# Optimization experiments

Hardware: AMD Instinct MI355X
Metric: run time of the kernel (lower is better)

Reference implementation:

```python
import jax, jax.numpy as jnp
import numpy as np

D_MODEL = 1024
NUM_HEADS = 16
DK = D_MODEL // NUM_HEADS
THETA = 10000.0
B, S = 4, 2048


def _rope(x, pos):
    # x: [B, H, S, dk], pos: [S] int positions
    half = DK // 2
    inv_freq = THETA ** (-jnp.arange(half, dtype=jnp.float32) * 2.0 / DK)  # [half]
    ang = pos.astype(jnp.float32)[:, None] * inv_freq[None, :]             # [S, half]
    cos, sin = jnp.cos(ang), jnp.sin(ang)                                  # [S, half]
    x_even = x[..., 0::2]
    x_odd = x[..., 1::2]
    out_even = x_even * cos - x_odd * sin
    out_odd = x_even * sin + x_odd * cos
    # interleave back to [..., dk]
    return jnp.stack([out_even, out_odd], axis=-1).reshape(x.shape)


def setup_inputs() -> dict:
    key = jax.random.key(0)
    ks = jax.random.split(key, 5)
    scale = 1.0 / np.sqrt(D_MODEL)
    return {
        "x": jax.random.normal(ks[0], (B, S, D_MODEL), dtype=jnp.float32),
        "token_position": jnp.arange(S, dtype=jnp.int32),
        "wq": jax.random.normal(ks[1], (D_MODEL, D_MODEL), dtype=jnp.float32) * scale,
        "wk": jax.random.normal(ks[2], (D_MODEL, D_MODEL), dtype=jnp.float32) * scale,
        "wv": jax.random.normal(ks[3], (D_MODEL, D_MODEL), dtype=jnp.float32) * scale,
        "wo": jax.random.normal(ks[4], (D_MODEL, D_MODEL), dtype=jnp.float32) * scale,
    }


def reference(x, token_position, wq, wk, wv, wo):
    b, s, _ = x.shape
    # QKV projections (torch Linear: y = x @ W.T), split heads -> [B, H, S, dk]
    def proj(w):
        y = jnp.einsum("bsd,ed->bse", x, w)
        return y.reshape(b, s, NUM_HEADS, DK).transpose(0, 2, 1, 3)
    q, k, v = proj(wq), proj(wk), proj(wv)
    q = _rope(q, token_position)
    k = _rope(k, token_position)
    # causal SDPA
    scores = jnp.einsum("bhqd,bhkd->bhqk", q, k) / jnp.sqrt(jnp.float32(DK))
    causal = jnp.tril(jnp.ones((s, s), dtype=bool))
    scores = jnp.where(causal, scores, -jnp.inf)
    attn = jax.nn.softmax(scores, axis=-1)
    out = jnp.einsum("bhqk,bhkd->bhqd", attn, v)          # [B, H, S, dv]
    out = out.transpose(0, 2, 1, 3).reshape(b, s, D_MODEL)  # merge heads
    return jnp.einsum("bsd,ed->bse", out, wo)             # output projection
```

## Files before the change

### kernel.cpp

```cpp
#include <hip/hip_runtime.h>


#define D_MODEL 1024
#define NH      16
#define DKH     64
#define SEQ     2048
#define BATCH   4
#define SCALE_LOG2 0.180336875461f
#define ROPE_L2    0.41524101186092029f

typedef _Float16 f16;
typedef _Float16 f16x8 __attribute__((ext_vector_type(8)));
typedef _Float16 f16x4 __attribute__((ext_vector_type(4)));
typedef __fp16   fp16x2n __attribute__((ext_vector_type(2)));
typedef float    f32x4 __attribute__((ext_vector_type(4)));
typedef unsigned short u16;
typedef unsigned int   u32;

__device__ __forceinline__ void glds16(const void* g, void* l) {
  __builtin_amdgcn_global_load_lds((const __attribute__((address_space(1))) void*)g,
                                   (__attribute__((address_space(3))) void*)l, 16, 0, 0);
}
__device__ __forceinline__ u32 pk(float a, float b) {
  union { fp16x2n h; u32 u; } c; c.h = __builtin_amdgcn_cvt_pkrtz(a, b); return c.u;
}

#define VMW_(N) asm volatile("s_waitcnt vmcnt(" #N ")" ::: "memory")
#define VMW(N) VMW_(N)
#define BAR() __builtin_amdgcn_s_barrier()
#define PRE_MFMA() do {                                                       \
    __builtin_amdgcn_s_barrier();                                             \
    asm volatile("s_waitcnt lgkmcnt(0)" ::: "memory");                        \
    __builtin_amdgcn_sched_barrier(0);                                        \
  } while (0)

__global__ void cvt_all(const float* __restrict__ x,
                        const float* __restrict__ w0, const float* __restrict__ w1,
                        const float* __restrict__ w2, const float* __restrict__ w3,
                        f16* __restrict__ xo, f16* __restrict__ o0, f16* __restrict__ o1,
                        f16* __restrict__ o2, f16* __restrict__ o3) {
  int blk = blockIdx.x;
  const float* src; f16* dst; int off;
  if (blk < 8192) { src = x; dst = xo; off = blk; }
  else {
    int t = blk - 8192; int w = t >> 10; off = t & 1023;
    switch (w) { case 0: src = w0; dst = o0; break;  case 1: src = w1; dst = o1; break;
                 case 2: src = w2; dst = o2; break;  default: src = w3; dst = o3; break; }
  }
  int i = (off * 256 + threadIdx.x) * 4;
  float4 v = *(const float4*)(src + i);
  uint2 o; o.x = pk(v.x, v.y); o.y = pk(v.z, v.w);
  *(uint2*)(dst + i) = o;
}

__global__ __launch_bounds__(512, 2) void gemm_qkv(const f16* __restrict__ A,
                                                   const f16* __restrict__ W,
                                                   f16* __restrict__ Qo,
                                                   f16* __restrict__ Ko,
                                                   f16* __restrict__ Vo,
                                                   const int* __restrict__ pos) {
  extern __shared__ char lds[];
  const int bid  = blockIdx.x;
  const int lin  = (bid & 7) * 64 + (bid >> 3);
  const int bx   = lin & 15, by = lin >> 4;
  const int m0   = by * 256, n0 = bx * 192;
  const int tid  = threadIdx.x;
  const int wave = tid >> 6, lane = tid & 63;
  const int quad = lane >> 4, l16 = lane & 15;
  const int wr   = wave >> 2, wc = wave & 3;

  f32x4 acc[8][3];
#pragma unroll
  for (int i = 0; i < 8; ++i)
#pragma unroll
    for (int j = 0; j < 3; ++j) acc[i][j] = (f32x4){0.f, 0.f, 0.f, 0.f};

  const int posR = (l16 & 1) * 4 + (quad ^ ((l16 >> 1) & 3));
  const char* aRd  = lds + wr * 8192 + (l16 >> 1) * 128 + posR * 16;
  const char* bRd0 = lds + 65536 + (wc * 48 + l16) * 128 + ((quad) ^ (l16 & 7)) * 16;
  const char* bRd1 = lds + 65536 + (wc * 48 + l16) * 128 + ((4 + quad) ^ (l16 & 7)) * 16;

  const int srA = tid >> 3;
  const int rA  = 2 * srA + ((tid >> 2) & 1);
  const int cA  = (tid & 3) ^ (srA & 3);
  const f16* pA0 = A + (size_t)(m0 + rA) * 1024 + cA * 8;
  const f16* pA1 = pA0 + (size_t)128 * 1024;
  const int gB = (tid & 7) ^ ((tid >> 3) & 7);
  const f16* pB0 = W + (size_t)(n0 + (tid >> 3)) * 1024 + gB * 8;
  const f16* pB1 = pB0 + (size_t)64 * 1024;
  const f16* pB2 = pB0 + (size_t)128 * 1024;
  char* const sdA = lds + (size_t)(tid & 448) * 16;
  char* const sdB = lds + 65536 + (size_t)(tid & 448) * 16;

  f16x8 af[2][4];
  f16x8 bf[2][3];

#define ST_A(TB, H) do {                                                      \
    glds16(pA0 + (H) * 32, sdA + (TB) * 32768 + (H) * 16384);                 \
    glds16(pA1 + (H) * 32, sdA + (TB) * 32768 + (H) * 16384 + 8192);          \
  } while (0)
#define ST_B(TB) do {                                                         \
    glds16(pB0, sdB + (TB) * 24576);                                          \
    glds16(pB1, sdB + (TB) * 24576 + 8192);                                   \
    glds16(pB2, sdB + (TB) * 24576 + 16384);                                  \
  } while (0)
#define RDAF(S, BUF, H, MG) do { _Pragma("unroll")                            \
    for (int i_ = 0; i_ < 4; ++i_)                                            \
      af[S][i_] = *(const f16x8*)(aRd + (BUF) * 32768 + (H) * 16384 +         \
                                  (MG) * 4096 + i_ * 1024);                   \
  } while (0)
#define RDBF(S, BUF, H) do { _Pragma("unroll")                                \
    for (int j_ = 0; j_ < 3; ++j_)                                            \
      bf[S][j_] = *(const f16x8*)(((H) ? bRd1 : bRd0) + (BUF) * 24576 +       \
                                  j_ * 2048);                                 \
  } while (0)
#define MMQ(AS, BS, MG) do {                                                  \
    __builtin_amdgcn_s_setprio(1);                                            \
    _Pragma("unroll")                                                         \
    for (int i_ = 0; i_ < 4; ++i_) { _Pragma("unroll")                        \
      for (int j_ = 0; j_ < 3; ++j_)                                          \
        acc[(MG) * 4 + i_][j_] = __builtin_amdgcn_mfma_f32_16x16x32_f16(      \
            af[AS][i_], bf[BS][j_], acc[(MG) * 4 + i_][j_], 0, 0, 0); }       \
    __builtin_amdgcn_s_setprio(0);                                            \
  } while (0)

#define TILEQ(BUF, DS, V1, V3) do {                                           \
    RDAF(1, BUF, 0, 1);                                                       \
    if (DS) ST_A((BUF) ^ 1, 0);                                               \
    MMQ(0, 0, 0);                                                             \
    VMW(V1); BAR();                                                           \
    RDAF(0, BUF, 1, 0); RDBF(1, BUF, 1);                                      \
    if (DS) ST_B((BUF) ^ 1);                                                  \
    MMQ(1, 0, 1);                                                             \
    BAR();                                                                    \
    RDAF(1, BUF, 1, 1);                                                       \
    if (DS) ST_A((BUF) ^ 1, 1);                                               \
    MMQ(0, 1, 0);                                                             \
    VMW(V3); BAR();                                                           \
    RDAF(0, (BUF) ^ 1, 0, 0); RDBF(0, (BUF) ^ 1, 0);                          \
    MMQ(1, 1, 1);                                                             \
    if (DS) { pA0 += 64; pA1 += 64; pB0 += 64; pB1 += 64; pB2 += 64; }        \
  } while (0)

  ST_A(0, 0); ST_B(0); ST_A(0, 1);
  pA0 += 64; pA1 += 64; pB0 += 64; pB1 += 64; pB2 += 64;
  VMW_(2);
  BAR();
  RDAF(0, 0, 0, 0);
  RDBF(0, 0, 0);

#pragma unroll 1
  for (int it = 0; it < 7; ++it) {
    TILEQ(0, 1, 2, 2);
    TILEQ(1, 1, 2, 2);
  }
  TILEQ(0, 1, 2, 2);

  RDAF(1, 1, 0, 1);
  MMQ(0, 0, 0);
  VMW_(0); BAR();
  RDAF(0, 1, 1, 0); RDBF(1, 1, 1);
  MMQ(1, 0, 1);
  RDAF(1, 1, 1, 1);
  MMQ(0, 1, 0);
  MMQ(1, 1, 1);

#undef TILEQ
#undef MMQ
#undef RDBF
#undef RDAF
#undef ST_B
#undef ST_A

  f16* dsts[3]; int colB[3]; bool rp[3]; float invf[3], sgn[3];
#pragma unroll
  for (int ni = 0; ni < 3; ++ni) {
    int gc  = n0 + wc * 48 + ni * 16 + l16;
    int seg = gc >> 10;
    dsts[ni] = (seg == 0) ? Qo : (seg == 1) ? Ko : Vo;
    colB[ni] = gc & 1023;
    rp[ni]   = (seg < 2);
    int dk   = gc & 63;
    invf[ni] = __builtin_amdgcn_exp2f(-ROPE_L2 * (float)(dk >> 1));
    sgn[ni]  = (dk & 1) ? 1.f : -1.f;
  }
#pragma unroll
  for (int a = 0; a < 8; ++a)
#pragma unroll
    for (int r = 0; r < 4; ++r) {
      int row = m0 + wr * 128 + a * 16 + quad * 4 + r;
      float ps = (float)pos[row & (SEQ - 1)];
#pragma unroll
      for (int ni = 0; ni < 3; ++ni) {
        float v = acc[a][ni][r];
        float ov;
        if (rp[ni]) {
          float ang = ps * invf[ni];
          float c = __cosf(ang), sn = __sinf(ang);
          float p = __shfl_xor(v, 1);
          ov = fmaf(p * sgn[ni], sn, v * c);
        } else ov = v;
        dsts[ni][(size_t)row * 1024 + colB[ni]] = (f16)ov;
      }
    }
}

__global__ __launch_bounds__(512, 2) void gemm_out(const f16* __restrict__ A,
                                                   const f16* __restrict__ W,
                                                   float* __restrict__ C) {
  extern __shared__ char lds[];
  const int bid  = blockIdx.x;
  const int lin  = (bid & 7) * 32 + (bid >> 3);
  const int bx   = lin & 3, by = lin >> 2;
  const int m0   = by * 128, n0 = bx * 256;
  const int tid  = threadIdx.x;
  const int wave = tid >> 6, lane = tid & 63;
  const int quad = lane >> 4, l16 = lane & 15;
  const int wr   = wave >> 2, wc = wave & 3;

  f32x4 acc[4][4];
#pragma unroll
  for (int i = 0; i < 4; ++i)
#pragma unroll
    for (int j = 0; j < 4; ++j) acc[i][j] = (f32x4){0.f, 0.f, 0.f, 0.f};

  const int posR = (l16 & 1) * 4 + (quad ^ ((l16 >> 1) & 3));
  const char* aRd = lds + wr * 4096 + (l16 >> 1) * 128 + posR * 16;
  const char* bRd = lds + 32768 + wc * 4096 + (l16 >> 1) * 128 + posR * 16;

  const int srA = tid >> 3;
  const int rA  = 2 * srA + ((tid >> 2) & 1);
  const int cA  = (tid & 3) ^ (srA & 3);
  const f16* pA = A + (size_t)(m0 + rA) * 1024 + cA * 8;
  const int rB  = 2 * (tid >> 3) + ((tid >> 2) & 1);
  const int cB  = (tid & 3) ^ ((tid >> 3) & 3);
  const f16* pB0 = W + (size_t)(n0 + rB) * 1024 + cB * 8;
  const f16* pB1 = pB0 + (size_t)128 * 1024;
  char* const sdA = lds + (size_t)(tid & 448) * 16;
  char* const sdB = lds + 32768 + (size_t)(tid & 448) * 16;

#define ST_AO(TB, H) glds16(pA + (H) * 32, sdA + (TB) * 16384 + (H) * 8192)
#define ST_BO(TB, H) do {                                                     \
    glds16(pB0 + (H) * 32, sdB + (TB) * 32768 + (H) * 16384);                 \
    glds16(pB1 + (H) * 32, sdB + (TB) * 32768 + (H) * 16384 + 8192);          \
  } while (0)
#define HALF(BUF, H, DOSTAGE, VMN, LAST) do {                                 \
    f16x8 af[4], bf[4];                                                       \
    _Pragma("unroll")                                                         \
    for (int i_ = 0; i_ < 4; ++i_)                                            \
      af[i_] = *(const f16x8*)(aRd + (BUF) * 16384 + (H) * 8192 + i_ * 1024); \
    _Pragma("unroll")                                                         \
    for (int j_ = 0; j_ < 4; ++j_)                                            \
      bf[j_] = *(const f16x8*)(bRd + (BUF) * 32768 + (H) * 16384 + j_ * 1024);\
    if (DOSTAGE) { ST_AO((BUF) ^ 1, H); ST_BO((BUF) ^ 1, H); }                \
    PRE_MFMA();                                                               \
    __builtin_amdgcn_s_setprio(1);                                            \
    _Pragma("unroll")                                                         \
    for (int i_ = 0; i_ < 4; ++i_) { _Pragma("unroll")                        \
      for (int j_ = 0; j_ < 4; ++j_)                                          \
        acc[i_][j_] = __builtin_amdgcn_mfma_f32_16x16x32_f16(                 \
            af[i_], bf[j_], acc[i_][j_], 0, 0, 0); }                          \
    __builtin_amdgcn_s_setprio(0);                                            \
    if (!(LAST)) {                                                            \
      VMW(VMN); __builtin_amdgcn_sched_barrier(0);                            \
      __builtin_amdgcn_s_barrier();                                           \
    }                                                                         \
  } while (0)

  ST_AO(0, 0); ST_BO(0, 0); ST_AO(0, 1); ST_BO(0, 1);
  pA += 64; pB0 += 64; pB1 += 64;
  VMW_(3); __builtin_amdgcn_sched_barrier(0);
  __builtin_amdgcn_s_barrier();

#pragma unroll 1
  for (int it = 0; it < 7; ++it) {
    HALF(0, 0, 1, 3, 0); HALF(0, 1, 1, 3, 0); pA += 64; pB0 += 64; pB1 += 64;
    HALF(1, 0, 1, 3, 0); HALF(1, 1, 1, 3, 0); pA += 64; pB0 += 64; pB1 += 64;
  }
  HALF(0, 0, 1, 3, 0); HALF(0, 1, 1, 3, 0);
  HALF(1, 0, 0, 0, 0);
  HALF(1, 1, 0, 0, 1);

#undef HALF
#undef ST_BO
#undef ST_AO

  float* dst = C;
#pragma unroll
  for (int a = 0; a < 4; ++a)
#pragma unroll
    for (int ni = 0; ni < 4; ++ni)
#pragma unroll
      for (int r = 0; r < 4; ++r) {
        int row = m0 + wr * 64 + a * 16 + quad * 4 + r;
        int col = n0 + wc * 64 + ni * 16 + l16;
        dst[(size_t)row * 1024 + col] = acc[a][ni][r];
      }
}

__global__ __launch_bounds__(256, 3) void flash_attn(const f16* __restrict__ Q,
                                                     const f16* __restrict__ Kg,
                                                     const f16* __restrict__ Vg,
                                                     f16* __restrict__ O) {
  __shared__ char smem[38400];
  f16*  KsL         = (f16*)smem;
  u32   (*Vt)[67]   = (u32(*)[67])(smem + 16384);
  float (*Red0)[66] = (float(*)[66])smem;
  float (*Red1)[66] = (float(*)[66])(smem + 16896);
  float (*Lb)[17]   = (float(*)[17])(smem + 33792);

  const int tid  = threadIdx.x;
  const int bh   = blockIdx.x;
  const int b    = bh >> 4, h = bh & 15;
  const int qblk = 31 - (int)blockIdx.y;
  const int q0   = qblk * 64;
  const int wave = tid >> 6, lane = tid & 63;
  const int quad = lane >> 4, l16 = lane & 15;
  const int nkt  = (qblk + 2) >> 1;

  f16x8 qf[4][2];
#pragma unroll
  for (int nt = 0; nt < 4; ++nt)
#pragma unroll
    for (int ks = 0; ks < 2; ++ks) {
      f16x8 qv = *(const f16x8*)(Q + ((size_t)(b * SEQ + q0 + nt * 16 + l16)) * D_MODEL
                                   + h * DKH + ks * 32 + quad * 8);
      qf[nt][ks] = qv * (f16)SCALE_LOG2;
    }

  f32x4 o[4][4];
#pragma unroll
  for (int md = 0; md < 4; ++md)
#pragma unroll
    for (int nt = 0; nt < 4; ++nt) o[md][nt] = (f32x4){0.f, 0.f, 0.f, 0.f};
  float lacc[4] = {0.f, 0.f, 0.f, 0.f};

  const int kp = tid >> 3, dc = (tid & 7) * 8;

  for (int t = 0; t < nkt; ++t) {
    const int kt = t * 128;
    const f16* vb = Vg + ((size_t)(b * SEQ + kt + 2 * kp)) * D_MODEL + h * DKH + dc;
    uint4 v0 = *(const uint4*)vb;
    uint4 v1 = *(const uint4*)(vb + D_MODEL);
    uint4 v2 = *(const uint4*)(vb + 64 * D_MODEL);
    uint4 v3 = *(const uint4*)(vb + 65 * D_MODEL);

    if (t) __syncthreads();
#pragma unroll
    for (int i = 0; i < 4; ++i) {
      int ci = i * 256 + tid;
      int row = ci >> 3, gc = (ci & 7) ^ (row & 7);
      glds16(Kg + ((size_t)(b * SEQ + kt + row)) * D_MODEL + h * DKH + gc * 8,
             smem + (size_t)(i * 256 + (tid & 192)) * 16);
    }
    {
      union { uint4 u; u16 s[8]; } a0, a1, a2, a3;
      a0.u = v0; a1.u = v1; a2.u = v2; a3.u = v3;
#pragma unroll
      for (int j = 0; j < 8; ++j) {
        Vt[dc + j][kp]      = (u32)a0.s[j] | ((u32)a1.s[j] << 16);
        Vt[dc + j][32 + kp] = (u32)a2.s[j] | ((u32)a3.s[j] << 16);
      }
    }
    __syncthreads();

    f16x4 pb[2][4];
#pragma unroll
    for (int mt = 0; mt < 2; ++mt) {
      const int krow = wave * 32 + mt * 16 + l16;
      const int s0 = quad ^ (krow & 7);
      f16x8 ka0 = *(const f16x8*)(KsL + krow * 64 + s0 * 8);
      f16x8 ka1 = *(const f16x8*)(KsL + krow * 64 + (s0 ^ 4) * 8);
      const int keyb = kt + wave * 32 + mt * 16 + quad * 4;
#pragma unroll
      for (int nt = 0; nt < 4; ++nt) {
        f32x4 c = (f32x4){0.f, 0.f, 0.f, 0.f};
        c = __builtin_amdgcn_mfma_f32_16x16x32_f16(ka0, qf[nt][0], c, 0, 0, 0);
        c = __builtin_amdgcn_mfma_f32_16x16x32_f16(ka1, qf[nt][1], c, 0, 0, 0);
        const int q = q0 + nt * 16 + l16;
        float p0 = __builtin_amdgcn_exp2f(c[0]);
        float p1 = __builtin_amdgcn_exp2f(c[1]);
        float p2 = __builtin_amdgcn_exp2f(c[2]);
        float p3 = __builtin_amdgcn_exp2f(c[3]);
        if (t == nkt - 1) {
          p0 = (keyb + 0 <= q) ? p0 : 0.f;
          p1 = (keyb + 1 <= q) ? p1 : 0.f;
          p2 = (keyb + 2 <= q) ? p2 : 0.f;
          p3 = (keyb + 3 <= q) ? p3 : 0.f;
        }
        lacc[nt] += (p0 + p1) + (p2 + p3);
        union { u32 w[2]; f16x4 v; } pp;
        pp.w[0] = pk(p0, p1); pp.w[1] = pk(p2, p3);
        pb[mt][nt] = pp.v;
      }
    }

#pragma unroll
    for (int md = 0; md < 4; ++md)
#pragma unroll
      for (int ks2 = 0; ks2 < 2; ++ks2) {
        const u32* vp = &Vt[md * 16 + l16][wave * 16 + ks2 * 8 + quad * 2];
        union { u32 x[2]; f16x4 v; } va;
        va.x[0] = vp[0]; va.x[1] = vp[1];
#pragma unroll
        for (int nt = 0; nt < 4; ++nt)
          o[md][nt] = __builtin_amdgcn_mfma_f32_16x16x16f16(va.v, pb[ks2][nt], o[md][nt], 0, 0, 0);
      }
  }

  __syncthreads();
  {
    float (*Rw)[66] = (wave >= 2) ? Red1 : Red0;
    if ((wave & 1) == 0) {
#pragma unroll
      for (int md = 0; md < 4; ++md)
#pragma unroll
        for (int nt = 0; nt < 4; ++nt)
#pragma unroll
          for (int r = 0; r < 4; ++r)
            Rw[md * 16 + quad * 4 + r][nt * 16 + l16] = o[md][nt][r];
    }
#pragma unroll
    for (int nt = 0; nt < 4; ++nt)
      Lb[nt * 16 + l16][wave * 4 + quad] = lacc[nt];
    __syncthreads();
    if (wave & 1) {
#pragma unroll
      for (int md = 0; md < 4; ++md)
#pragma unroll
        for (int nt = 0; nt < 4; ++nt)
#pragma unroll
          for (int r = 0; r < 4; ++r)
            Rw[md * 16 + quad * 4 + r][nt * 16 + l16] += o[md][nt][r];
    }
    __syncthreads();
  }

  {
    const int q = tid & 63, dc4 = (tid >> 6) * 16;
    float lsum = 0.f;
#pragma unroll
    for (int j = 0; j < 16; ++j) lsum += Lb[q][j];
    float linv = __builtin_amdgcn_rcpf(lsum);
    union { uint4 u[2]; u32 w[8]; } ov;
#pragma unroll
    for (int i = 0; i < 8; ++i) {
      float f0 = Red0[dc4 + 2 * i][q]     + Red1[dc4 + 2 * i][q];
      float f1 = Red0[dc4 + 2 * i + 1][q] + Red1[dc4 + 2 * i + 1][q];
      ov.w[i] = pk(f0 * linv, f1 * linv);
    }
    f16* op = O + ((size_t)(b * SEQ + q0 + q)) * D_MODEL + h * DKH + dc4;
    *(uint4*)op = ov.u[0];
    *(uint4*)(op + 8) = ov.u[1];
  }
}

extern "C" void kernel_launch(void* const* d_in, const int* in_sizes, int n_in,
                              void* d_out, int out_size, void* d_ws, size_t ws_size,
                              hipStream_t stream) {
  const float* x      = (const float*)d_in[0];
  const int*   tokpos = (const int*)d_in[1];
  const float* wq     = (const float*)d_in[2];
  const float* wk     = (const float*)d_in[3];
  const float* wv     = (const float*)d_in[4];
  const float* wo     = (const float*)d_in[5];
  float* out = (float*)d_out;

  char* ws = (char*)d_ws;
  f16* Xb  = (f16*)(ws + 0);
  f16* Wqb = (f16*)(ws + 16777216);
  f16* Wkb = (f16*)(ws + 18874368);
  f16* Wvb = (f16*)(ws + 20971520);
  f16* Wob = (f16*)(ws + 23068672);
  f16* Qb  = (f16*)(ws + 25165824);
  f16* Kb  = (f16*)(ws + 41943040);
  f16* Vb  = (f16*)(ws + 58720256);
  f16* Ob  = Xb;

  static bool attr_done = false;
  if (!attr_done) {
    (void)hipFuncSetAttribute(reinterpret_cast<const void*>(gemm_qkv),
                              hipFuncAttributeMaxDynamicSharedMemorySize, 114688);
    (void)hipFuncSetAttribute(reinterpret_cast<const void*>(gemm_out),
                              hipFuncAttributeMaxDynamicSharedMemorySize, 98304);
    attr_done = true;
  }

  cvt_all<<<12288, 256, 0, stream>>>(x, wq, wk, wv, wo, Xb, Wqb, Wkb, Wvb, Wob);

  gemm_qkv<<<512, 512, 114688, stream>>>(Xb, Wqb, Qb, Kb, Vb, tokpos);

  flash_attn<<<dim3(BATCH * NH, 32), 256, 0, stream>>>(Qb, Kb, Vb, Ob);

  gemm_out<<<256, 512, 98304, stream>>>(Ob, Wob, out);
}
```

Before: 246.9 us.

## Restructure output-projection GEMM to 256x128 tiles with register double-buffered fragments

```diff
diff --git a/kernel.cpp b/kernel.cpp
--- a/kernel.cpp
+++ b/kernel.cpp
@@ -28,11 +28,6 @@
 #define VMW_(N) asm volatile("s_waitcnt vmcnt(" #N ")" ::: "memory")
 #define VMW(N) VMW_(N)
 #define BAR() __builtin_amdgcn_s_barrier()
-#define PRE_MFMA() do {                                                       \
-    __builtin_amdgcn_s_barrier();                                             \
-    asm volatile("s_waitcnt lgkmcnt(0)" ::: "memory");                        \
-    __builtin_amdgcn_sched_barrier(0);                                        \
-  } while (0)
 
 __global__ void cvt_all(const float* __restrict__ x,
                         const float* __restrict__ w0, const float* __restrict__ w1,
@@ -211,90 +206,123 @@
   extern __shared__ char lds[];
   const int bid  = blockIdx.x;
   const int lin  = (bid & 7) * 32 + (bid >> 3);
-  const int bx   = lin & 3, by = lin >> 2;
-  const int m0   = by * 128, n0 = bx * 256;
+  const int bx   = lin & 7, by = lin >> 3;
+  const int m0   = by * 256, n0 = bx * 128;
   const int tid  = threadIdx.x;
   const int wave = tid >> 6, lane = tid & 63;
   const int quad = lane >> 4, l16 = lane & 15;
   const int wr   = wave >> 2, wc = wave & 3;
 
-  f32x4 acc[4][4];
-#pragma unroll
-  for (int i = 0; i < 4; ++i)
-#pragma unroll
-    for (int j = 0; j < 4; ++j) acc[i][j] = (f32x4){0.f, 0.f, 0.f, 0.f};
+  f32x4 acc[8][2];
+#pragma unroll
+  for (int i = 0; i < 8; ++i)
+#pragma unroll
+    for (int j = 0; j < 2; ++j) acc[i][j] = (f32x4){0.f, 0.f, 0.f, 0.f};
 
   const int posR = (l16 & 1) * 4 + (quad ^ ((l16 >> 1) & 3));
-  const char* aRd = lds + wr * 4096 + (l16 >> 1) * 128 + posR * 16;
-  const char* bRd = lds + 32768 + wc * 4096 + (l16 >> 1) * 128 + posR * 16;
+  const char* aRd  = lds + wr * 8192 + (l16 >> 1) * 128 + posR * 16;
+  const char* bRd0 = lds + 65536 + (wc * 32 + l16) * 128 + ((quad) ^ (l16 & 7)) * 16;
+  const char* bRd1 = lds + 65536 + (wc * 32 + l16) * 128 + ((4 + quad) ^ (l16 & 7)) * 16;
 
   const int srA = tid >> 3;
   const int rA  = 2 * srA + ((tid >> 2) & 1);
   const int cA  = (tid & 3) ^ (srA & 3);
-  const f16* pA = A + (size_t)(m0 + rA) * 1024 + cA * 8;
-  const int rB  = 2 * (tid >> 3) + ((tid >> 2) & 1);
-  const int cB  = (tid & 3) ^ ((tid >> 3) & 3);
-  const f16* pB0 = W + (size_t)(n0 + rB) * 1024 + cB * 8;
-  const f16* pB1 = pB0 + (size_t)128 * 1024;
+  const f16* pA0 = A + (size_t)(m0 + rA) * 1024 + cA * 8;
+  const f16* pA1 = pA0 + (size_t)128 * 1024;
+  const int gB = (tid & 7) ^ ((tid >> 3) & 7);
+  const f16* pB0 = W + (size_t)(n0 + (tid >> 3)) * 1024 + gB * 8;
+  const f16* pB1 = pB0 + (size_t)64 * 1024;
   char* const sdA = lds + (size_t)(tid & 448) * 16;
-  char* const sdB = lds + 32768 + (size_t)(tid & 448) * 16;
-
-#define ST_AO(TB, H) glds16(pA + (H) * 32, sdA + (TB) * 16384 + (H) * 8192)
-#define ST_BO(TB, H) do {                                                     \
-    glds16(pB0 + (H) * 32, sdB + (TB) * 32768 + (H) * 16384);                 \
-    glds16(pB1 + (H) * 32, sdB + (TB) * 32768 + (H) * 16384 + 8192);          \
-  } while (0)
-#define HALF(BUF, H, DOSTAGE, VMN, LAST) do {                                 \
-    f16x8 af[4], bf[4];                                                       \
-    _Pragma("unroll")                                                         \
+  char* const sdB = lds + 65536 + (size_t)(tid & 448) * 16;
+
+  f16x8 af[2][4];
+  f16x8 bf[2][2];
+
+#define ST_A(TB, H) do {                                                      \
+    glds16(pA0 + (H) * 32, sdA + (TB) * 32768 + (H) * 16384);                 \
+    glds16(pA1 + (H) * 32, sdA + (TB) * 32768 + (H) * 16384 + 8192);          \
+  } while (0)
+#define ST_B(TB) do {                                                         \
+    glds16(pB0, sdB + (TB) * 16384);                                          \
+    glds16(pB1, sdB + (TB) * 16384 + 8192);                                   \
+  } while (0)
+#define RDAF(S, BUF, H, MG) do { _Pragma("unroll")                            \
     for (int i_ = 0; i_ < 4; ++i_)                                            \
-      af[i_] = *(const f16x8*)(aRd + (BUF) * 16384 + (H) * 8192 + i_ * 1024); \
-    _Pragma("unroll")                                                         \
-    for (int j_ = 0; j_ < 4; ++j_)                                            \
-      bf[j_] = *(const f16x8*)(bRd + (BUF) * 32768 + (H) * 16384 + j_ * 1024);\
-    if (DOSTAGE) { ST_AO((BUF) ^ 1, H); ST_BO((BUF) ^ 1, H); }                \
-    PRE_MFMA();                                                               \
+      af[S][i_] = *(const f16x8*)(aRd + (BUF) * 32768 + (H) * 16384 +         \
+                                  (MG) * 4096 + i_ * 1024);                   \
+  } while (0)
+#define RDBF(S, BUF, H) do { _Pragma("unroll")                                \
+    for (int j_ = 0; j_ < 2; ++j_)                                            \
+      bf[S][j_] = *(const f16x8*)(((H) ? bRd1 : bRd0) + (BUF) * 16384 +       \
+                                  j_ * 2048);                                 \
+  } while (0)
+#define MMQ(AS, BS, MG) do {                                                  \
     __builtin_amdgcn_s_setprio(1);                                            \
     _Pragma("unroll")                                                         \
     for (int i_ = 0; i_ < 4; ++i_) { _Pragma("unroll")                        \
-      for (int j_ = 0; j_ < 4; ++j_)                                          \
-        acc[i_][j_] = __builtin_amdgcn_mfma_f32_16x16x32_f16(                 \
-            af[i_], bf[j_], acc[i_][j_], 0, 0, 0); }                          \
+      for (int j_ = 0; j_ < 2; ++j_)                                          \
+        acc[(MG) * 4 + i_][j_] = __builtin_amdgcn_mfma_f32_16x16x32_f16(      \
+            af[AS][i_], bf[BS][j_], acc[(MG) * 4 + i_][j_], 0, 0, 0); }       \
     __builtin_amdgcn_s_setprio(0);                                            \
-    if (!(LAST)) {                                                            \
-      VMW(VMN); __builtin_amdgcn_sched_barrier(0);                            \
-      __builtin_amdgcn_s_barrier();                                           \
-    }                                                                         \
-  } while (0)
-
-  ST_AO(0, 0); ST_BO(0, 0); ST_AO(0, 1); ST_BO(0, 1);
-  pA += 64; pB0 += 64; pB1 += 64;
-  VMW_(3); __builtin_amdgcn_sched_barrier(0);
-  __builtin_amdgcn_s_barrier();
+  } while (0)
+
+#define TILEO(BUF, DS, V1, V3) do {                                           \
+    RDAF(1, BUF, 0, 1);                                                       \
+    if (DS) ST_A((BUF) ^ 1, 0);                                               \
+    MMQ(0, 0, 0);                                                             \
+    VMW(V1); BAR();                                                           \
+    RDAF(0, BUF, 1, 0); RDBF(1, BUF, 1);                                      \
+    if (DS) ST_B((BUF) ^ 1);                                                  \
+    MMQ(1, 0, 1);                                                             \
+    BAR();                                                                    \
+    RDAF(1, BUF, 1, 1);                                                       \
+    if (DS) ST_A((BUF) ^ 1, 1);                                               \
+    MMQ(0, 1, 0);                                                             \
+    VMW(V3); BAR();                                                           \
+    RDAF(0, (BUF) ^ 1, 0, 0); RDBF(0, (BUF) ^ 1, 0);                          \
+    MMQ(1, 1, 1);                                                             \
+    if (DS) { pA0 += 64; pA1 += 64; pB0 += 64; pB1 += 64; }                   \
+  } while (0)
+
+  ST_A(0, 0); ST_B(0); ST_A(0, 1);
+  pA0 += 64; pA1 += 64; pB0 += 64; pB1 += 64;
+  VMW_(2);
+  BAR();
+  RDAF(0, 0, 0, 0);
+  RDBF(0, 0, 0);
 
 #pragma unroll 1
   for (int it = 0; it < 7; ++it) {
-    HALF(0, 0, 1, 3, 0); HALF(0, 1, 1, 3, 0); pA += 64; pB0 += 64; pB1 += 64;
-    HALF(1, 0, 1, 3, 0); HALF(1, 1, 1, 3, 0); pA += 64; pB0 += 64; pB1 += 64;
-  }
-  HALF(0, 0, 1, 3, 0); HALF(0, 1, 1, 3, 0);
-  HALF(1, 0, 0, 0, 0);
-  HALF(1, 1, 0, 0, 1);
-
-#undef HALF
-#undef ST_BO
-#undef ST_AO
-
-  float* dst = C;
-#pragma unroll
-  for (int a = 0; a < 4; ++a)
-#pragma unroll
-    for (int ni = 0; ni < 4; ++ni)
+    TILEO(0, 1, 2, 2);
+    TILEO(1, 1, 2, 2);
+  }
+  TILEO(0, 1, 2, 2);
+
+  RDAF(1, 1, 0, 1);
+  MMQ(0, 0, 0);
+  VMW_(0); BAR();
+  RDAF(0, 1, 1, 0); RDBF(1, 1, 1);
+  MMQ(1, 0, 1);
+  RDAF(1, 1, 1, 1);
+  MMQ(0, 1, 0);
+  MMQ(1, 1, 1);
+
+#undef TILEO
+#undef MMQ
+#undef RDBF
+#undef RDAF
+#undef ST_B
+#undef ST_A
+
+#pragma unroll
+  for (int a = 0; a < 8; ++a)
+#pragma unroll
+    for (int ni = 0; ni < 2; ++ni)
 #pragma unroll
       for (int r = 0; r < 4; ++r) {
-        int row = m0 + wr * 64 + a * 16 + quad * 4 + r;
-        int col = n0 + wc * 64 + ni * 16 + l16;
-        dst[(size_t)row * 1024 + col] = acc[a][ni][r];
+        int row = m0 + wr * 128 + a * 16 + quad * 4 + r;
+        int col = n0 + wc * 32 + ni * 16 + l16;
+        C[(size_t)row * 1024 + col] = acc[a][ni][r];
       }
 }
 
```

After: 252.2 us. 1.02x slower.
